# Kernel tuning notes

Hardware: AMD Instinct MI355X
Metric: run time of the kernel (lower is better)

## Reference

```python
import jax, jax.numpy as jnp
import numpy as np

N_NODES = 100000
N_EDGES = 1600000
D_IN = 128
D_OUT = 128


def setup_inputs() -> dict:
    key = jax.random.key(0)
    k1, k2, k3, k4 = jax.random.split(key, 4)
    feat = jax.random.normal(k1, (N_NODES, D_IN), dtype=jnp.float32)
    # xavier_uniform on [D_IN, D_OUT]
    limit = float(np.sqrt(6.0 / (D_IN + D_OUT)))
    weight = jax.random.uniform(k2, (D_IN, D_OUT), minval=-limit, maxval=limit, dtype=jnp.float32)
    bias = jnp.zeros((D_OUT,), dtype=jnp.float32)
    src = jax.random.randint(k3, (N_EDGES,), 0, N_NODES, dtype=jnp.int32)
    dst = jax.random.randint(k4, (N_EDGES,), 0, N_NODES, dtype=jnp.int32)
    return {"feat": feat, "weight": weight, "bias": bias, "src": src, "dst": dst}


def reference(feat, weight, bias, src, dst):
    n = feat.shape[0]
    # in-degree of each node (number of incoming edges)
    deg = jax.ops.segment_sum(jnp.ones_like(dst, dtype=feat.dtype), dst, num_segments=n)
    norm = jnp.power(jnp.clip(deg, 1.0), -0.5)[:, None]  # [N, 1]
    # pre-normalize source features
    h = feat * norm
    # copy_src + sum aggregation: scatter-add messages from src to dst
    agg = jax.ops.segment_sum(h[src], dst, num_segments=n)  # [N, D_IN]
    # in_feats == out_feats -> matmul after aggregation (the else-branch)
    rst = jnp.matmul(agg, weight)
    rst = rst * norm + bias
    return rst
```

## Files before the change

### kernel.cpp

```cpp
#include <hip/hip_runtime.h>

#define D 128
#define BSHIFT 9
#define BNODES 512
#define BMASK 511
#define NB_MAX 256
#define STRIDE 10240
#define BIN_CHUNK 4096

typedef unsigned int uint;
typedef __attribute__((ext_vector_type(8))) short bf16x8;
typedef __attribute__((ext_vector_type(4))) float f32x4;

__device__ inline uint bf16_rne(float x) {
    uint u = __float_as_uint(x);
    return (u + 0x7fffu + ((u >> 16) & 1u)) >> 16;
}
__device__ inline uint pack2(float lo, float hi) {
    return bf16_rne(lo) | (bf16_rne(hi) << 16);
}

__global__ void __launch_bounds__(256) bin_kernel(const int* __restrict__ src,
                                                  const int* __restrict__ dst,
                                                  int* __restrict__ bucket_cur,
                                                  uint* __restrict__ binned,
                                                  int n_edges) {
    __shared__ int h[NB_MAX];
    __shared__ int base[NB_MAX];
    int t = threadIdx.x;
    long long e0 = (long long)blockIdx.x * BIN_CHUNK;
    h[t] = 0;
    __syncthreads();

    int d[16], s[16];
#pragma unroll
    for (int k = 0; k < 16; ++k) {
        long long idx = e0 + k * 256 + t;
        if (idx < n_edges) {
            d[k] = dst[idx];
            s[k] = src[idx];
            atomicAdd(&h[d[k] >> BSHIFT], 1);
        } else {
            d[k] = -1;
        }
    }
    __syncthreads();
    {
        int c = h[t];
        base[t] = c ? atomicAdd(&bucket_cur[t], c) : 0;
        h[t] = 0;
    }
    __syncthreads();
#pragma unroll
    for (int k = 0; k < 16; ++k) {
        if (d[k] >= 0) {
            int b = d[k] >> BSHIFT;
            int r = base[b] + atomicAdd(&h[b], 1);
            if (r < STRIDE)
                binned[(size_t)b * STRIDE + r] =
                    ((uint)s[k] << BSHIFT) | (uint)(d[k] & BMASK);
        }
    }
}

__global__ void __launch_bounds__(BNODES) fill2_kernel(
        const int* __restrict__ bucket_cur, uint* __restrict__ csr,
        float* __restrict__ norm, int* __restrict__ row_start,
        int* __restrict__ degp, int n_nodes) {
    __shared__ uint sbin[STRIDE];
    __shared__ int deg[BNODES];
    __shared__ int rs[BNODES];
    __shared__ int cur[BNODES];
    int b = blockIdx.x;
    int t = threadIdx.x;
    int cnt = bucket_cur[b];
    if (cnt > STRIDE) cnt = STRIDE;
    size_t gbase = (size_t)b * STRIDE;

    for (int k = t; k < cnt; k += BNODES) sbin[k] = csr[gbase + k];
    deg[t] = 0;
    __syncthreads();
    for (int k = t; k < cnt; k += BNODES) atomicAdd(&deg[sbin[k] & BMASK], 1);
    __syncthreads();

    int v = deg[t];
    rs[t] = v;
    __syncthreads();
    for (int o = 1; o < BNODES; o <<= 1) {
        int a = (t >= o) ? rs[t - o] : 0;
        __syncthreads();
        rs[t] += a;
        __syncthreads();
    }
    int excl = rs[t] - v;
    __syncthreads();
    rs[t] = excl;
    cur[t] = 0;

    int node = b * BNODES + t;
    if (node < n_nodes) {
        row_start[node] = (int)gbase + excl;
        degp[node] = v;
        norm[node] = rsqrtf(fmaxf((float)v, 1.0f));
    }
    __syncthreads();

    for (int k = t; k < cnt; k += BNODES) {
        uint p = sbin[k];
        int dl = p & BMASK;
        int r = atomicAdd(&cur[dl], 1);
        csr[gbase + rs[dl] + r] = p >> BSHIFT;
    }
}

__global__ void __launch_bounds__(256) prep_kernel(
        const float* __restrict__ feat, const float* __restrict__ norm,
        uint* __restrict__ h32, int n_nodes) {
    long long idx = (long long)blockIdx.x * 256 + threadIdx.x;
    if (idx >= (long long)n_nodes * 32) return;
    int i = (int)(idx >> 5);
    float nm = norm[i];
    float4 f = *(const float4*)(feat + idx * 4);
    uint2 o;
    o.x = pack2(f.x * nm, f.y * nm);
    o.y = pack2(f.z * nm, f.w * nm);
    *(uint2*)(h32 + idx * 2) = o;
}

__global__ void prep_w_kernel(const float* __restrict__ W,
                              uint4* __restrict__ wpack) {
    int idx = blockIdx.x * 256 + threadIdx.x;
    if (idx >= 2048) return;
    int lane = idx & 63;
    int ks = (idx >> 6) & 3;
    int ct = idx >> 8;
    int col = ct * 16 + (lane & 15);
    int k0 = ks * 32 + (lane >> 4) * 8;
    uint4 u;
    u.x = pack2(W[(k0 + 0) * D + col], W[(k0 + 1) * D + col]);
    u.y = pack2(W[(k0 + 2) * D + col], W[(k0 + 3) * D + col]);
    u.z = pack2(W[(k0 + 4) * D + col], W[(k0 + 5) * D + col]);
    u.w = pack2(W[(k0 + 6) * D + col], W[(k0 + 7) * D + col]);
    wpack[idx] = u;
}

#define UNPACK_ADD(u)                              \
    acc[0] += __uint_as_float((u).x << 16);        \
    acc[1] += __uint_as_float((u).x & 0xffff0000u);\
    acc[2] += __uint_as_float((u).y << 16);        \
    acc[3] += __uint_as_float((u).y & 0xffff0000u);\
    acc[4] += __uint_as_float((u).z << 16);        \
    acc[5] += __uint_as_float((u).z & 0xffff0000u);\
    acc[6] += __uint_as_float((u).w << 16);        \
    acc[7] += __uint_as_float((u).w & 0xffff0000u);

__global__ void __launch_bounds__(256) gather_kernel(
        const uint4* __restrict__ h128, const uint* __restrict__ csr,
        const int* __restrict__ row_start, const int* __restrict__ degp,
        float* __restrict__ agg, int n_nodes) {
    int lane = threadIdx.x & 63;
    int wid = threadIdx.x >> 6;
    int i = blockIdx.x * 4 + wid;
    if (i >= n_nodes) return;
    int beg = row_start[i];
    int end = beg + degp[i];
    int g = lane >> 4;
    int c = lane & 15;
    float acc[8];
#pragma unroll
    for (int j = 0; j < 8; ++j) acc[j] = 0.f;

    for (int base = beg; base < end; base += 64) {
        int nk = end - base;
        if (nk > 64) nk = 64;
        int epre = (base + lane < end) ? (int)csr[base + lane] : 0;
        int k = 0;
        int kfull = nk & ~7;
        for (; k < kfull; k += 8) {
            int s0 = __shfl(epre, k + g, 64);
            int s1 = __shfl(epre, k + 4 + g, 64);
            uint4 u0 = h128[(size_t)s0 * 16 + c];
            uint4 u1 = h128[(size_t)s1 * 16 + c];
            UNPACK_ADD(u0);
            UNPACK_ADD(u1);
        }
        if (k < nk) {
            int e0 = k + g;
            int e1 = k + 4 + g;
            int s0 = __shfl(epre, e0 & 63, 64);
            int s1 = __shfl(epre, e1 & 63, 64);
            uint4 z = {0u, 0u, 0u, 0u};
            uint4 u0 = (e0 < nk) ? h128[(size_t)s0 * 16 + c] : z;
            uint4 u1 = (e1 < nk) ? h128[(size_t)s1 * 16 + c] : z;
            UNPACK_ADD(u0);
            UNPACK_ADD(u1);
        }
    }

#pragma unroll
    for (int j = 0; j < 8; ++j) {
        acc[j] += __shfl_xor(acc[j], 16, 64);
        acc[j] += __shfl_xor(acc[j], 32, 64);
    }
    if (g == 0) {
        float4* orow = (float4*)(agg + (size_t)i * D);
        float4 lo = {acc[0], acc[1], acc[2], acc[3]};
        float4 hi = {acc[4], acc[5], acc[6], acc[7]};
        orow[2 * c] = lo;
        orow[2 * c + 1] = hi;
    }
}

__global__ void __launch_bounds__(256) mm_mfma_kernel(
        float* __restrict__ io, const uint4* __restrict__ wpack,
        const float* __restrict__ bias, const float* __restrict__ norm, int n) {
    int t = threadIdx.x;
    int lane = t & 63;
    int w = t >> 6;
    int r0 = blockIdx.x * 64 + w * 16;
    int g = lane >> 4;

    int arow = r0 + (lane & 15);
    int arow_c = arow < n ? arow : n - 1;
    const float* ap = io + (size_t)arow_c * D + g * 8;

    uint4 afr[4];
#pragma unroll
    for (int ks = 0; ks < 4; ++ks) {
        float4 f0 = *(const float4*)(ap + ks * 32);
        float4 f1 = *(const float4*)(ap + ks * 32 + 4);
        afr[ks].x = pack2(f0.x, f0.y);
        afr[ks].y = pack2(f0.z, f0.w);
        afr[ks].z = pack2(f1.x, f1.y);
        afr[ks].w = pack2(f1.z, f1.w);
    }

    float nm[4];
    int orow[4];
#pragma unroll
    for (int r = 0; r < 4; ++r) {
        orow[r] = r0 + g * 4 + r;
        int rc = orow[r] < n ? orow[r] : n - 1;
        nm[r] = norm[rc];
    }

    int col = lane & 15;
#pragma unroll
    for (int ct = 0; ct < 8; ++ct) {
        f32x4 acc = {0.f, 0.f, 0.f, 0.f};
#pragma unroll
        for (int ks = 0; ks < 4; ++ks) {
            uint4 bu = wpack[(ct * 4 + ks) * 64 + lane];
            acc = __builtin_amdgcn_mfma_f32_16x16x32_bf16(
                *(bf16x8*)&afr[ks], *(bf16x8*)&bu, acc, 0, 0, 0);
        }
        float bv = bias[ct * 16 + col];
#pragma unroll
        for (int r = 0; r < 4; ++r)
            if (orow[r] < n)
                io[(size_t)orow[r] * D + ct * 16 + col] = acc[r] * nm[r] + bv;
    }
}

extern "C" void kernel_launch(void* const* d_in, const int* in_sizes, int n_in,
                              void* d_out, int out_size, void* d_ws, size_t ws_size,
                              hipStream_t stream) {
    const float* feat   = (const float*)d_in[0];
    const float* weight = (const float*)d_in[1];
    const float* bias   = (const float*)d_in[2];
    const int*   src    = (const int*)d_in[3];
    const int*   dst    = (const int*)d_in[4];
    float* out = (float*)d_out;

    int n_nodes = in_sizes[0] / D;
    int n_edges = in_sizes[3];
    int nb = (n_nodes + BNODES - 1) >> BSHIFT;

    float* norm       = (float*)d_ws;
    int*   degp       = (int*)(norm + n_nodes);
    int*   row_start  = degp + n_nodes;
    int*   bucket_cur = row_start + n_nodes;
    uint*  csr        = (uint*)(bucket_cur + NB_MAX);
    uint*  h32        = csr + (size_t)nb * STRIDE;
    uint4* wpack      = (uint4*)(h32 + (size_t)n_nodes * 64);

    hipMemsetAsync(bucket_cur, 0, NB_MAX * sizeof(int), stream);

    bin_kernel<<<(n_edges + BIN_CHUNK - 1) / BIN_CHUNK, 256, 0, stream>>>(
        src, dst, bucket_cur, csr, n_edges);
    fill2_kernel<<<nb, BNODES, 0, stream>>>(bucket_cur, csr, norm, row_start,
                                            degp, n_nodes);
    prep_w_kernel<<<8, 256, 0, stream>>>(weight, wpack);
    prep_kernel<<<(n_nodes * 32 + 255) / 256, 256, 0, stream>>>(feat, norm, h32,
                                                                n_nodes);
    gather_kernel<<<(n_nodes + 3) / 4, 256, 0, stream>>>((const uint4*)h32, csr,
                                                         row_start, degp, out,
                                                         n_nodes);
    mm_mfma_kernel<<<(n_nodes + 63) / 64, 256, 0, stream>>>(out, wpack, bias,
                                                            norm, n_nodes);
}
```

Baseline: 142.6 us.

## Fuse gather aggregation with MFMA matmul via shared-memory staging

Merges the gather kernel and the matmul kernel into one kernel. Each block aggregates 16 nodes into an LDS tile, then each wave computes two 16-column output tiles with MFMA. This removes the round trip of the fp32 aggregate through global memory and one kernel launch. In exchange, each wave processes four nodes sequentially, and the block waits on a barrier, so load imbalance across nodes can stall the matmul phase.

```diff
diff --git a/kernel.cpp b/kernel.cpp
--- a/kernel.cpp
+++ b/kernel.cpp
@@ -154,81 +154,78 @@
     acc[6] += __uint_as_float((u).w << 16);        \
     acc[7] += __uint_as_float((u).w & 0xffff0000u);
 
-__global__ void __launch_bounds__(256) gather_kernel(
+#define LDP 132
+
+__global__ void __launch_bounds__(256) gather_mm_kernel(
         const uint4* __restrict__ h128, const uint* __restrict__ csr,
         const int* __restrict__ row_start, const int* __restrict__ degp,
-        float* __restrict__ agg, int n_nodes) {
-    int lane = threadIdx.x & 63;
-    int wid = threadIdx.x >> 6;
-    int i = blockIdx.x * 4 + wid;
-    if (i >= n_nodes) return;
-    int beg = row_start[i];
-    int end = beg + degp[i];
-    int g = lane >> 4;
-    int c = lane & 15;
-    float acc[8];
-#pragma unroll
-    for (int j = 0; j < 8; ++j) acc[j] = 0.f;
-
-    for (int base = beg; base < end; base += 64) {
-        int nk = end - base;
-        if (nk > 64) nk = 64;
-        int epre = (base + lane < end) ? (int)csr[base + lane] : 0;
-        int k = 0;
-        int kfull = nk & ~7;
-        for (; k < kfull; k += 8) {
-            int s0 = __shfl(epre, k + g, 64);
-            int s1 = __shfl(epre, k + 4 + g, 64);
-            uint4 u0 = h128[(size_t)s0 * 16 + c];
-            uint4 u1 = h128[(size_t)s1 * 16 + c];
-            UNPACK_ADD(u0);
-            UNPACK_ADD(u1);
-        }
-        if (k < nk) {
-            int e0 = k + g;
-            int e1 = k + 4 + g;
-            int s0 = __shfl(epre, e0 & 63, 64);
-            int s1 = __shfl(epre, e1 & 63, 64);
-            uint4 z = {0u, 0u, 0u, 0u};
-            uint4 u0 = (e0 < nk) ? h128[(size_t)s0 * 16 + c] : z;
-            uint4 u1 = (e1 < nk) ? h128[(size_t)s1 * 16 + c] : z;
-            UNPACK_ADD(u0);
-            UNPACK_ADD(u1);
-        }
-    }
-
-#pragma unroll
-    for (int j = 0; j < 8; ++j) {
-        acc[j] += __shfl_xor(acc[j], 16, 64);
-        acc[j] += __shfl_xor(acc[j], 32, 64);
-    }
-    if (g == 0) {
-        float4* orow = (float4*)(agg + (size_t)i * D);
-        float4 lo = {acc[0], acc[1], acc[2], acc[3]};
-        float4 hi = {acc[4], acc[5], acc[6], acc[7]};
-        orow[2 * c] = lo;
-        orow[2 * c + 1] = hi;
-    }
-}
-
-__global__ void __launch_bounds__(256) mm_mfma_kernel(
-        float* __restrict__ io, const uint4* __restrict__ wpack,
-        const float* __restrict__ bias, const float* __restrict__ norm, int n) {
+        const float* __restrict__ norm, const uint4* __restrict__ wpack,
+        const float* __restrict__ bias, float* __restrict__ out, int n) {
+    __shared__ float As[16][LDP];
     int t = threadIdx.x;
     int lane = t & 63;
     int w = t >> 6;
-    int r0 = blockIdx.x * 64 + w * 16;
+    int r0 = blockIdx.x * 16;
     int g = lane >> 4;
-
-    int arow = r0 + (lane & 15);
-    int arow_c = arow < n ? arow : n - 1;
-    const float* ap = io + (size_t)arow_c * D + g * 8;
+    int c = lane & 15;
+
+    for (int q = 0; q < 4; ++q) {
+        int local = w * 4 + q;
+        int i = r0 + local;
+        float acc[8];
+#pragma unroll
+        for (int j = 0; j < 8; ++j) acc[j] = 0.f;
+
+        if (i < n) {
+            int beg = row_start[i];
+            int end = beg + degp[i];
+            for (int base = beg; base < end; base += 64) {
+                int nk = end - base;
+                if (nk > 64) nk = 64;
+                int epre = (base + lane < end) ? (int)csr[base + lane] : 0;
+                int k = 0;
+                int kfull = nk & ~7;
+                for (; k < kfull; k += 8) {
+                    int s0 = __shfl(epre, k + g, 64);
+                    int s1 = __shfl(epre, k + 4 + g, 64);
+                    uint4 u0 = h128[(size_t)s0 * 16 + c];
+                    uint4 u1 = h128[(size_t)s1 * 16 + c];
+                    UNPACK_ADD(u0);
+                    UNPACK_ADD(u1);
+                }
+                if (k < nk) {
+                    int e0 = k + g;
+                    int e1 = k + 4 + g;
+                    int s0 = __shfl(epre, e0 & 63, 64);
+                    int s1 = __shfl(epre, e1 & 63, 64);
+                    uint4 z = {0u, 0u, 0u, 0u};
+                    uint4 u0 = (e0 < nk) ? h128[(size_t)s0 * 16 + c] : z;
+                    uint4 u1 = (e1 < nk) ? h128[(size_t)s1 * 16 + c] : z;
+                    UNPACK_ADD(u0);
+                    UNPACK_ADD(u1);
+                }
+            }
+        }
+#pragma unroll
+        for (int j = 0; j < 8; ++j) {
+            acc[j] += __shfl_xor(acc[j], 16, 64);
+            acc[j] += __shfl_xor(acc[j], 32, 64);
+        }
+        if (g == 0) {
+            float4 lo = {acc[0], acc[1], acc[2], acc[3]};
+            float4 hi = {acc[4], acc[5], acc[6], acc[7]};
+            *(float4*)&As[local][8 * c] = lo;
+            *(float4*)&As[local][8 * c + 4] = hi;
+        }
+    }
+    __syncthreads();
 
     uint4 afr[4];
 #pragma unroll
     for (int ks = 0; ks < 4; ++ks) {
-        float4 f0 = *(const float4*)(ap + ks * 32);
-        float4 f1 = *(const float4*)(ap + ks * 32 + 4);
+        const float* ap = &As[c][ks * 32 + g * 8];
+        float4 f0 = *(const float4*)ap;
+        float4 f1 = *(const float4*)(ap + 4);
         afr[ks].x = pack2(f0.x, f0.y);
         afr[ks].y = pack2(f0.z, f0.w);
         afr[ks].z = pack2(f1.x, f1.y);
@@ -236,17 +233,17 @@
     }
 
     float nm[4];
-    int orow[4];
+    int grow[4];
 #pragma unroll
     for (int r = 0; r < 4; ++r) {
-        orow[r] = r0 + g * 4 + r;
-        int rc = orow[r] < n ? orow[r] : n - 1;
+        grow[r] = r0 + g * 4 + r;
+        int rc = grow[r] < n ? grow[r] : n - 1;
         nm[r] = norm[rc];
     }
 
-    int col = lane & 15;
-#pragma unroll
-    for (int ct = 0; ct < 8; ++ct) {
+#pragma unroll
+    for (int cc = 0; cc < 2; ++cc) {
+        int ct = 2 * w + cc;
         f32x4 acc = {0.f, 0.f, 0.f, 0.f};
 #pragma unroll
         for (int ks = 0; ks < 4; ++ks) {
@@ -254,11 +251,11 @@
             acc = __builtin_amdgcn_mfma_f32_16x16x32_bf16(
                 *(bf16x8*)&afr[ks], *(bf16x8*)&bu, acc, 0, 0, 0);
         }
-        float bv = bias[ct * 16 + col];
+        float bv = bias[ct * 16 + c];
 #pragma unroll
         for (int r = 0; r < 4; ++r)
-            if (orow[r] < n)
-                io[(size_t)orow[r] * D + ct * 16 + col] = acc[r] * nm[r] + bv;
+            if (grow[r] < n)
+                out[(size_t)grow[r] * D + ct * 16 + c] = acc[r] * nm[r] + bv;
     }
 }
 
@@ -293,9 +290,6 @@
     prep_w_kernel<<<8, 256, 0, stream>>>(weight, wpack);
     prep_kernel<<<(n_nodes * 32 + 255) / 256, 256, 0, stream>>>(feat, norm, h32,
                                                                 n_nodes);
-    gather_kernel<<<(n_nodes + 3) / 4, 256, 0, stream>>>((const uint4*)h32, csr,
-                                                         row_start, degp, out,
-                                                         n_nodes);
-    mm_mfma_kernel<<<(n_nodes + 63) / 64, 256, 0, stream>>>(out, wpack, bias,
-                                                            norm, n_nodes);
-}
+    gather_mm_kernel<<<(n_nodes + 15) / 16, 256, 0, stream>>>(
+        (const uint4*)h32, csr, row_start, degp, norm, wpack, bias, out, n_nodes);
+}
```

Measured after the change: 132.8 us. -6.9%, faster.
